# Kernel optimization log

Hardware: AMD Instinct MI355X
Metric: run time of the kernel (lower is better)

## Reference

```python
import jax, jax.numpy as jnp
import numpy as np

B, N = 65536, 8
OBS0, OBS1, OBS2 = 6, 1024, 7
H, HC, NA = 64, 128, 2


def _glorot(key, shape):
    fan_in = shape[0]
    lim = 1.0 / np.sqrt(fan_in)
    return jax.random.uniform(key, shape, jnp.float32, -lim, lim)


def setup_inputs() -> dict:
    key = jax.random.key(0)
    ks = jax.random.split(key, 24)
    state0 = jax.random.normal(ks[0], (B, OBS0), jnp.float32)
    state1 = jax.random.normal(ks[1], (B, OBS1), jnp.float32)
    state2 = jax.random.normal(ks[2], (B, N, OBS2), jnp.float32)
    keep = (jax.random.uniform(ks[3], (B, N, 1)) > 0.35) | (jnp.arange(N)[None, :, None] == 0)
    state2 = state2 * keep.astype(jnp.float32)
    return {
        "state0": state0, "state1": state1, "state2": state2,
        "W0": _glorot(ks[4], (OBS0, H)), "b0": jnp.zeros((H,), jnp.float32),
        "Wg": _glorot(ks[5], (OBS1, H)), "bg": jnp.zeros((H,), jnp.float32),
        "Ws1": _glorot(ks[6], (OBS2, H)), "bs1": jnp.zeros((H,), jnp.float32),
        "Ws2": _glorot(ks[7], (H, H)), "bs2": jnp.zeros((H,), jnp.float32),
        "Wq": _glorot(ks[8], (H, H)),
        "Wk": _glorot(ks[9], (H, H)),
        "Wv": _glorot(ks[10], (H, H)),
        "Wc1": _glorot(ks[11], (3 * H, HC)), "bc1": jnp.zeros((HC,), jnp.float32),
        "Wc2": _glorot(ks[12], (HC, HC)), "bc2": jnp.zeros((HC,), jnp.float32),
        "Wc3": _glorot(ks[13], (HC, NA)), "bc3": jnp.zeros((NA,), jnp.float32),
    }


def reference(state0, state1, state2,
              W0, b0, Wg, bg, Ws1, bs1, Ws2, bs2,
              Wq, Wk, Wv, Wc1, bc1, Wc2, bc2, Wc3, bc3):
    own_e = jax.nn.relu(state0 @ W0 + b0)                      # [B, 64]
    env_e = jax.nn.relu(state1 @ Wg + bg)                      # [B, 64]
    intru_e = jax.nn.relu(state2 @ Ws1 + bs1)                  # [B, N, 64]
    intru_e = jax.nn.relu(intru_e @ Ws2 + bs2)                 # [B, N, 64]

    q = own_e @ Wq                                             # [B, 64]
    k = intru_e @ Wk                                           # [B, N, 64]
    v = intru_e @ Wv                                           # [B, N, 64]

    # mask: True where the neighbor slot is non-padding (mean over feats != 0)
    mask = jnp.mean(state2, axis=2, keepdims=True) != 0        # [B, N, 1] bool

    score = jnp.einsum('bnd,bd->bn', k, q)[..., None]          # [B, N, 1]
    score_m = jnp.where(mask, score, -jnp.inf)
    alpha = jax.nn.softmax(score_m / np.sqrt(H), axis=1)       # [B, N, 1]
    alpha_m = jnp.where(mask, alpha, 0.0)
    v_att = jnp.sum(v * alpha_m, axis=1)                       # [B, 64]

    concat = jnp.concatenate((own_e, env_e, v_att), axis=1)    # [B, 192]
    h = jax.nn.relu(concat @ Wc1 + bc1)
    h = jax.nn.relu(h @ Wc2 + bc2)
    return jnp.tanh(h @ Wc3 + bc3)                             # [B, n_actions]
```

## Files before the change

### kernel.cpp

```cpp
#include <hip/hip_runtime.h>
#include <math.h>


typedef float f32x4 __attribute__((ext_vector_type(4)));
typedef __bf16 bf16x8 __attribute__((ext_vector_type(8)));
typedef unsigned short u16x8 __attribute__((ext_vector_type(8)));

#define DI __device__ __forceinline__

DI unsigned short f2bf_u(float f) {
  unsigned u = __builtin_bit_cast(unsigned, f);
  u += 0x7fffu + ((u >> 16) & 1u);
  return (unsigned short)(u >> 16);
}
DI float bfu2f(unsigned short s) {
  unsigned u = ((unsigned)s) << 16;
  return __builtin_bit_cast(float, u);
}
DI f32x4 mfma16(u16x8 a, u16x8 b, f32x4 c) {
  return __builtin_amdgcn_mfma_f32_16x16x32_bf16(
      __builtin_bit_cast(bf16x8, a), __builtin_bit_cast(bf16x8, b), c, 0, 0, 0);
}


constexpr size_t WS_ENV = 0;
constexpr size_t WS_WGF = 8388608;
constexpr size_t WS_WS2 = 8519680;
constexpr size_t WS_WV  = 8527872;
constexpr size_t WS_MQK = 8536064;
constexpr size_t WS_WC1 = 8544256;
constexpr size_t WS_WC2 = 8593408;
constexpr size_t WS_M32 = 8626176;

__global__ __launch_bounds__(256) void k_mqk(const float* __restrict__ Wq,
                                             const float* __restrict__ Wk,
                                             float* __restrict__ mqk) {
  const int idx = blockIdx.x * 256 + threadIdx.x;
  const int i = idx >> 6, h = idx & 63;
  const float* qp = Wq + i * 64;
  const float* kp = Wk + h * 64;
  float acc = 0.f;
#pragma unroll 16
  for (int d = 0; d < 64; ++d) acc = fmaf(qp[d], kp[d], acc);
  mqk[idx] = acc;
}

__global__ __launch_bounds__(256) void k_pack(
    const float* __restrict__ Wg, const float* __restrict__ Ws2,
    const float* __restrict__ Wv, const float* __restrict__ mqk,
    const float* __restrict__ Wc1, const float* __restrict__ Wc2,
    unsigned short* __restrict__ wgf, unsigned short* __restrict__ ws2f,
    unsigned short* __restrict__ wvf, unsigned short* __restrict__ mqkf,
    unsigned short* __restrict__ wc1f, unsigned short* __restrict__ wc2f) {
  const int idx = blockIdx.x * 256 + threadIdx.x;
  const float* src;
  unsigned short* dst;
  int i, ntm, NC;
  if (idx < 65536)      { src = Wg;  dst = wgf;  i = idx;          ntm = 2; NC = 64;  }
  else if (idx < 69632) { src = Ws2; dst = ws2f; i = idx - 65536;  ntm = 2; NC = 64;  }
  else if (idx < 73728) { src = Wv;  dst = wvf;  i = idx - 69632;  ntm = 2; NC = 64;  }
  else if (idx < 77824) { src = mqk; dst = mqkf; i = idx - 73728;  ntm = 2; NC = 64;  }
  else if (idx < 102400){ src = Wc1; dst = wc1f; i = idx - 77824;  ntm = 3; NC = 128; }
  else                  { src = Wc2; dst = wc2f; i = idx - 102400; ntm = 3; NC = 128; }
  const int j = i & 7, ln = (i >> 3) & 63, t2 = i >> 9;
  const int nt = t2 & ((1 << ntm) - 1), kt = t2 >> ntm;
  const int k = kt * 32 + (ln >> 4) * 8 + j, n = nt * 16 + (ln & 15);
  dst[i] = f2bf_u(src[k * NC + n]);
}

__global__ __launch_bounds__(256) void k_env(const float* __restrict__ s1,
                                             const float* __restrict__ bg,
                                             const unsigned short* __restrict__ wgf,
                                             unsigned short* __restrict__ env) {
  const int lane = threadIdx.x & 63, wave = threadIdx.x >> 6;
  const int lo = lane & 15, q = lane >> 4;
  const int row16 = blockIdx.x * 64 + wave * 16;
  const float* arow = s1 + (size_t)(row16 + lo) * 1024 + q * 8;
  const u16x8* wp = (const u16x8*)wgf + lane;

  f32x4 acc0 = {}, acc1 = {}, acc2 = {}, acc3 = {};
  f32x4 a0 = *(const f32x4*)(arow);
  f32x4 a1 = *(const f32x4*)(arow + 4);
  u16x8 b0 = wp[0], b1 = wp[64], b2 = wp[128], b3 = wp[192];

  for (int ks = 0; ks < 32; ++ks) {
    const f32x4 ca0 = a0, ca1 = a1;
    const u16x8 cb0 = b0, cb1 = b1, cb2 = b2, cb3 = b3;
    if (ks < 31) {
      const float* ap = arow + (ks + 1) * 32;
      a0 = *(const f32x4*)ap;
      a1 = *(const f32x4*)(ap + 4);
      const u16x8* bp = wp + (size_t)(ks + 1) * 256;
      b0 = bp[0]; b1 = bp[64]; b2 = bp[128]; b3 = bp[192];
    }
    u16x8 af;
    af[0] = f2bf_u(ca0[0]); af[1] = f2bf_u(ca0[1]);
    af[2] = f2bf_u(ca0[2]); af[3] = f2bf_u(ca0[3]);
    af[4] = f2bf_u(ca1[0]); af[5] = f2bf_u(ca1[1]);
    af[6] = f2bf_u(ca1[2]); af[7] = f2bf_u(ca1[3]);
    acc0 = mfma16(af, cb0, acc0);
    acc1 = mfma16(af, cb1, acc1);
    acc2 = mfma16(af, cb2, acc2);
    acc3 = mfma16(af, cb3, acc3);
  }
  const float bias[4] = {bg[lo], bg[16 + lo], bg[32 + lo], bg[48 + lo]};
  const f32x4 av[4] = {acc0, acc1, acc2, acc3};
#pragma unroll
  for (int nt = 0; nt < 4; ++nt)
#pragma unroll
    for (int ri = 0; ri < 4; ++ri) {
      float v = fmaxf(av[nt][ri] + bias[nt], 0.f);
      env[(size_t)(row16 + q * 4 + ri) * 64 + nt * 16 + lo] = f2bf_u(v);
    }
}

__global__ __launch_bounds__(256) void k_fused(
    const float* __restrict__ s0, const float* __restrict__ s2,
    const unsigned short* __restrict__ env,
    const float* __restrict__ W0, const float* __restrict__ b0v,
    const float* __restrict__ Ws1, const float* __restrict__ bs1,
    const unsigned short* __restrict__ ws2f, const float* __restrict__ bs2,
    const unsigned short* __restrict__ wvf, const unsigned short* __restrict__ mqkf,
    const unsigned short* __restrict__ wc1f, const float* __restrict__ bc1,
    const unsigned short* __restrict__ wc2f, const float* __restrict__ bc2,
    const float* __restrict__ Wc3, const float* __restrict__ bc3,
    float* __restrict__ out) {
  __shared__ __align__(16) char smem[55296];
  u16x8* EF = (u16x8*)smem;
  unsigned short* EFs = (unsigned short*)smem;
  u16x8* H1F = (u16x8*)smem;
  unsigned short* H1Fs = (unsigned short*)smem;
  float* H2 = (float*)(smem + 8192);
  u16x8* CF = (u16x8*)(smem + 32768);
  unsigned short* CFs = (unsigned short*)(smem + 32768);
  float* QK = (float*)(smem + 45056);
  u16x8* SEF = (u16x8*)(smem + 45056);
  float* SC = (float*)(smem + 53248);
  float* AL = (float*)(smem + 54272);

  const int tid = threadIdx.x;
  const int lane = tid & 63, wave = tid >> 6;
  const int lo = lane & 15, q = lane >> 4;
  const int bbase = blockIdx.x * 32;

  bool maskreg;
  {
    const int r = tid, bl = r >> 3, n = r & 7;
    const float* x = s2 + ((size_t)(bbase + bl) * 8 + n) * 7;
    float xv[7];
#pragma unroll
    for (int j = 0; j < 7; ++j) xv[j] = x[j];
    float sum = 0.f;
#pragma unroll
    for (int j = 0; j < 7; ++j) sum += xv[j];
    maskreg = (sum != 0.f);
    const int mt = r >> 4, rl = r & 15;
#pragma unroll
    for (int c = 0; c < 8; ++c) {
      float a[8];
#pragma unroll
      for (int i = 0; i < 8; ++i) a[i] = bs1[c * 8 + i];
#pragma unroll
      for (int j = 0; j < 7; ++j) {
        const float* wr = Ws1 + j * 64 + c * 8;
#pragma unroll
        for (int i = 0; i < 8; ++i) a[i] = fmaf(xv[j], wr[i], a[i]);
      }
      u16x8 pk;
#pragma unroll
      for (int i = 0; i < 8; ++i) pk[i] = f2bf_u(fmaxf(a[i], 0.f));
      EF[(mt * 2 + (c >> 2)) * 64 + (((c & 3) << 4) | rl)] = pk;
    }
  }
  __syncthreads();

  {
    u16x8 Bf[4][2];
#pragma unroll
    for (int nt = 0; nt < 4; ++nt)
#pragma unroll
      for (int kt = 0; kt < 2; ++kt)
        Bf[nt][kt] = ((const u16x8*)ws2f)[(kt * 4 + nt) * 64 + lane];
    float bias[4];
#pragma unroll
    for (int nt = 0; nt < 4; ++nt) bias[nt] = bs2[nt * 16 + lo];
#pragma unroll
    for (int mi = 0; mi < 4; ++mi) {
      const int mt = wave * 4 + mi;
      const u16x8 A0 = EF[(mt * 2 + 0) * 64 + lane];
      const u16x8 A1 = EF[(mt * 2 + 1) * 64 + lane];
      f32x4 acc[4] = {};
#pragma unroll
      for (int nt = 0; nt < 4; ++nt) {
        acc[nt] = mfma16(A0, Bf[nt][0], acc[nt]);
        acc[nt] = mfma16(A1, Bf[nt][1], acc[nt]);
      }
#pragma unroll
      for (int nt = 0; nt < 4; ++nt) {
        const int h = nt * 16 + lo;
#pragma unroll
        for (int ri = 0; ri < 4; ++ri) {
          const float v = fmaxf(acc[nt][ri] + bias[nt], 0.f);
          const int rr = mt * 16 + q * 4 + ri;
          EFs[((mt * 2 + (h >> 5)) * 64 + ((((h >> 3) & 3) << 4) | (rr & 15))) * 8 +
              (h & 7)] = f2bf_u(v);
        }
      }
    }
  }
  __syncthreads();

  {
    const int bl = tid >> 3, c = tid & 7;
    const int mt = bl >> 4, fl = ((c & 3) << 4) | (bl & 15), kt = c >> 2;
    const float* x = s0 + (size_t)(bbase + bl) * 6;
    float xv[6];
#pragma unroll
    for (int j = 0; j < 6; ++j) xv[j] = x[j];
    float a[8];
#pragma unroll
    for (int i = 0; i < 8; ++i) a[i] = b0v[c * 8 + i];
#pragma unroll
    for (int j = 0; j < 6; ++j) {
      const float* wr = W0 + j * 64 + c * 8;
#pragma unroll
      for (int i = 0; i < 8; ++i) a[i] = fmaf(xv[j], wr[i], a[i]);
    }
    u16x8 pk;
#pragma unroll
    for (int i = 0; i < 8; ++i) pk[i] = f2bf_u(fmaxf(a[i], 0.f));
    CF[(mt * 6 + kt) * 64 + fl] = pk;
    const u16x8 ev = *(const u16x8*)(env + (size_t)(bbase + bl) * 64 + c * 8);
    CF[(mt * 6 + 2 + kt) * 64 + fl] = ev;
  }
  __syncthreads();

  {
#pragma unroll
    for (int pp = 0; pp < 2; ++pp) {
      const int p = wave * 2 + pp, mt = p >> 2, nt = p & 3;
      const u16x8 A0 = CF[(mt * 6 + 0) * 64 + lane];
      const u16x8 A1 = CF[(mt * 6 + 1) * 64 + lane];
      const u16x8 B0 = ((const u16x8*)mqkf)[(0 * 4 + nt) * 64 + lane];
      const u16x8 B1 = ((const u16x8*)mqkf)[(1 * 4 + nt) * 64 + lane];
      f32x4 acc = {};
      acc = mfma16(A0, B0, acc);
      acc = mfma16(A1, B1, acc);
#pragma unroll
      for (int ri = 0; ri < 4; ++ri)
        QK[(mt * 16 + q * 4 + ri) * 64 + nt * 16 + lo] = acc[ri];
    }
  }
  __syncthreads();

  {
    const int r = tid, bl = r >> 3, mt = r >> 4, rl = r & 15;
    float dot = 0.f;
#pragma unroll
    for (int c = 0; c < 8; ++c) {
      const u16x8 e = EF[(mt * 2 + (c >> 2)) * 64 + (((c & 3) << 4) | rl)];
      const float* qkp = QK + bl * 64 + c * 8;
      const f32x4 qa = *(const f32x4*)(qkp);
      const f32x4 qb = *(const f32x4*)(qkp + 4);
#pragma unroll
      for (int i = 0; i < 4; ++i) dot = fmaf(bfu2f(e[i]), qa[i], dot);
#pragma unroll
      for (int i = 0; i < 4; ++i) dot = fmaf(bfu2f(e[4 + i]), qb[i], dot);
    }
    SC[r] = maskreg ? dot * 0.125f : -1e30f;
  }
  __syncthreads();

  if (tid < 32) {
    float s[8];
#pragma unroll
    for (int n = 0; n < 8; ++n) s[n] = SC[tid * 8 + n];
    float mx = s[0];
#pragma unroll
    for (int n = 1; n < 8; ++n) mx = fmaxf(mx, s[n]);
    float e[8], sum = 0.f;
#pragma unroll
    for (int n = 0; n < 8; ++n) { e[n] = __expf(s[n] - mx); sum += e[n]; }
    const float inv = 1.f / sum;
#pragma unroll
    for (int n = 0; n < 8; ++n) AL[tid * 8 + n] = e[n] * inv;
  }
  __syncthreads();

  {
    const int bl = tid >> 3, c = tid & 7;
    float al[8];
#pragma unroll
    for (int n = 0; n < 8; ++n) al[n] = AL[bl * 8 + n];
    float a[8] = {0.f, 0.f, 0.f, 0.f, 0.f, 0.f, 0.f, 0.f};
#pragma unroll
    for (int n = 0; n < 8; ++n) {
      const int rr = bl * 8 + n;
      const u16x8 e =
          EF[((rr >> 4) * 2 + (c >> 2)) * 64 + (((c & 3) << 4) | (rr & 15))];
#pragma unroll
      for (int i = 0; i < 8; ++i) a[i] = fmaf(al[n], bfu2f(e[i]), a[i]);
    }
    u16x8 pk;
#pragma unroll
    for (int i = 0; i < 8; ++i) pk[i] = f2bf_u(a[i]);
    SEF[((bl >> 4) * 2 + (c >> 2)) * 64 + (((c & 3) << 4) | (bl & 15))] = pk;
  }
  __syncthreads();

  {
#pragma unroll
    for (int pp = 0; pp < 2; ++pp) {
      const int p = wave * 2 + pp, mt = p >> 2, nt = p & 3;
      const u16x8 A0 = SEF[(mt * 2 + 0) * 64 + lane];
      const u16x8 A1 = SEF[(mt * 2 + 1) * 64 + lane];
      const u16x8 B0 = ((const u16x8*)wvf)[(0 * 4 + nt) * 64 + lane];
      const u16x8 B1 = ((const u16x8*)wvf)[(1 * 4 + nt) * 64 + lane];
      f32x4 acc = {};
      acc = mfma16(A0, B0, acc);
      acc = mfma16(A1, B1, acc);
      const int h = nt * 16 + lo;
#pragma unroll
      for (int ri = 0; ri < 4; ++ri) {
        const int rr = mt * 16 + q * 4 + ri;
        CFs[((mt * 6 + 4 + (h >> 5)) * 64 + ((((h >> 3) & 3) << 4) | (rr & 15))) * 8 +
            (h & 7)] = f2bf_u(acc[ri]);
      }
    }
  }
  __syncthreads();

  {
    const int mt = wave & 1, ntb = (wave >> 1) * 4;
    u16x8 A[6];
#pragma unroll
    for (int kt = 0; kt < 6; ++kt) A[kt] = CF[(mt * 6 + kt) * 64 + lane];
#pragma unroll
    for (int ni = 0; ni < 4; ++ni) {
      const int nt = ntb + ni;
      f32x4 acc = {};
#pragma unroll
      for (int kt = 0; kt < 6; ++kt) {
        const u16x8 Bf = ((const u16x8*)wc1f)[(kt * 8 + nt) * 64 + lane];
        acc = mfma16(A[kt], Bf, acc);
      }
      const float bias = bc1[nt * 16 + lo];
      const int h = nt * 16 + lo;
#pragma unroll
      for (int ri = 0; ri < 4; ++ri) {
        const float v = fmaxf(acc[ri] + bias, 0.f);
        const int rr = mt * 16 + q * 4 + ri;
        H1Fs[((mt * 4 + (h >> 5)) * 64 + ((((h >> 3) & 3) << 4) | (rr & 15))) * 8 +
             (h & 7)] = f2bf_u(v);
      }
    }
  }
  __syncthreads();

  {
    const int mt = wave & 1, ntb = (wave >> 1) * 4;
    u16x8 A[4];
#pragma unroll
    for (int kt = 0; kt < 4; ++kt) A[kt] = H1F[(mt * 4 + kt) * 64 + lane];
#pragma unroll
    for (int ni = 0; ni < 4; ++ni) {
      const int nt = ntb + ni;
      f32x4 acc = {};
#pragma unroll
      for (int kt = 0; kt < 4; ++kt) {
        const u16x8 Bf = ((const u16x8*)wc2f)[(kt * 8 + nt) * 64 + lane];
        acc = mfma16(A[kt], Bf, acc);
      }
      const float bias = bc2[nt * 16 + lo];
#pragma unroll
      for (int ri = 0; ri < 4; ++ri)
        H2[(mt * 16 + q * 4 + ri) * 132 + nt * 16 + lo] =
            fmaxf(acc[ri] + bias, 0.f);
    }
  }
  __syncthreads();

  if (tid < 64) {
    const int bl = tid >> 1, a = tid & 1;
    float acc = bc3[a];
    const float* h2r = H2 + bl * 132;
#pragma unroll 8
    for (int h = 0; h < 128; ++h) acc = fmaf(h2r[h], Wc3[h * 2 + a], acc);
    out[(size_t)(bbase + bl) * 2 + a] = tanhf(acc);
  }
}

extern "C" void kernel_launch(void* const* d_in, const int* in_sizes, int n_in,
                              void* d_out, int out_size, void* d_ws, size_t ws_size,
                              hipStream_t stream) {
  const float* s0  = (const float*)d_in[0];
  const float* s1  = (const float*)d_in[1];
  const float* s2  = (const float*)d_in[2];
  const float* W0  = (const float*)d_in[3];
  const float* b0  = (const float*)d_in[4];
  const float* Wg  = (const float*)d_in[5];
  const float* bg  = (const float*)d_in[6];
  const float* Ws1 = (const float*)d_in[7];
  const float* bs1 = (const float*)d_in[8];
  const float* Ws2 = (const float*)d_in[9];
  const float* bs2 = (const float*)d_in[10];
  const float* Wq  = (const float*)d_in[11];
  const float* Wk  = (const float*)d_in[12];
  const float* Wv  = (const float*)d_in[13];
  const float* Wc1 = (const float*)d_in[14];
  const float* bc1 = (const float*)d_in[15];
  const float* Wc2 = (const float*)d_in[16];
  const float* bc2 = (const float*)d_in[17];
  const float* Wc3 = (const float*)d_in[18];
  const float* bc3 = (const float*)d_in[19];

  char* ws = (char*)d_ws;
  unsigned short* env  = (unsigned short*)(ws + WS_ENV);
  unsigned short* wgf  = (unsigned short*)(ws + WS_WGF);
  unsigned short* ws2f = (unsigned short*)(ws + WS_WS2);
  unsigned short* wvf  = (unsigned short*)(ws + WS_WV);
  unsigned short* mqkf = (unsigned short*)(ws + WS_MQK);
  unsigned short* wc1f = (unsigned short*)(ws + WS_WC1);
  unsigned short* wc2f = (unsigned short*)(ws + WS_WC2);
  float* mqk32 = (float*)(ws + WS_M32);

  hipLaunchKernelGGL(k_mqk, dim3(16), dim3(256), 0, stream, Wq, Wk, mqk32);
  hipLaunchKernelGGL(k_pack, dim3(464), dim3(256), 0, stream, Wg, Ws2, Wv, mqk32,
                     Wc1, Wc2, wgf, ws2f, wvf, mqkf, wc1f, wc2f);
  hipLaunchKernelGGL(k_env, dim3(1024), dim3(256), 0, stream, s1, bg, wgf, env);
  hipLaunchKernelGGL(k_fused, dim3(2048), dim3(256), 0, stream, s0, s2, env, W0,
                     b0, Ws1, bs1, ws2f, bs2, wvf, mqkf, wc1f, bc1, wc2f, bc2,
                     Wc3, bc3, (float*)d_out);
}
```

Before: 496.6 us.

## Fuse env GEMM into main kernel and merge mqk into weight packing

Moves the state1 @ Wg GEMM into the main per-block kernel, split-K across wave pairs with a shared-memory reduction, so the bf16 env intermediate is never written to or read back from global memory. The Wq·Wk^T product is computed inside the packing kernel, which removes one launch. Inputs are loaded up front, and the final Wc3 projection now uses all threads with shuffle reductions. The cost is higher register pressure in the fused kernel (launch bounds set to 3 blocks per CU), plus an extra barrier and shared-memory reduction step.

```diff
diff --git a/kernel.cpp b/kernel.cpp
--- a/kernel.cpp
+++ b/kernel.cpp
@@ -3,6 +3,8 @@
 
 
 typedef float f32x4 __attribute__((ext_vector_type(4)));
+typedef float f32x4u __attribute__((ext_vector_type(4), aligned(4)));
+typedef float f32x2u __attribute__((ext_vector_type(2), aligned(4)));
 typedef __bf16 bf16x8 __attribute__((ext_vector_type(8)));
 typedef unsigned short u16x8 __attribute__((ext_vector_type(8)));
 
@@ -17,115 +19,79 @@
   unsigned u = ((unsigned)s) << 16;
   return __builtin_bit_cast(float, u);
 }
+DI u16x8 cvt8(f32x4 x, f32x4 y) {
+  bf16x8 r;
+  r[0] = (__bf16)x[0]; r[1] = (__bf16)x[1]; r[2] = (__bf16)x[2]; r[3] = (__bf16)x[3];
+  r[4] = (__bf16)y[0]; r[5] = (__bf16)y[1]; r[6] = (__bf16)y[2]; r[7] = (__bf16)y[3];
+  return __builtin_bit_cast(u16x8, r);
+}
 DI f32x4 mfma16(u16x8 a, u16x8 b, f32x4 c) {
   return __builtin_amdgcn_mfma_f32_16x16x32_bf16(
       __builtin_bit_cast(bf16x8, a), __builtin_bit_cast(bf16x8, b), c, 0, 0, 0);
 }
 
 
-constexpr size_t WS_ENV = 0;
-constexpr size_t WS_WGF = 8388608;
-constexpr size_t WS_WS2 = 8519680;
-constexpr size_t WS_WV  = 8527872;
-constexpr size_t WS_MQK = 8536064;
-constexpr size_t WS_WC1 = 8544256;
-constexpr size_t WS_WC2 = 8593408;
-constexpr size_t WS_M32 = 8626176;
-
-__global__ __launch_bounds__(256) void k_mqk(const float* __restrict__ Wq,
-                                             const float* __restrict__ Wk,
-                                             float* __restrict__ mqk) {
-  const int idx = blockIdx.x * 256 + threadIdx.x;
-  const int i = idx >> 6, h = idx & 63;
-  const float* qp = Wq + i * 64;
-  const float* kp = Wk + h * 64;
-  float acc = 0.f;
-#pragma unroll 16
-  for (int d = 0; d < 64; ++d) acc = fmaf(qp[d], kp[d], acc);
-  mqk[idx] = acc;
-}
-
-__global__ __launch_bounds__(256) void k_pack(
+constexpr size_t WS_WGF = 0;
+constexpr size_t WS_WS2 = 131072;
+constexpr size_t WS_WV  = 139264;
+constexpr size_t WS_MQK = 147456;
+constexpr size_t WS_WC1 = 155648;
+constexpr size_t WS_WC2 = 204800;
+
+__global__ __launch_bounds__(256) void k_prep(
     const float* __restrict__ Wg, const float* __restrict__ Ws2,
-    const float* __restrict__ Wv, const float* __restrict__ mqk,
-    const float* __restrict__ Wc1, const float* __restrict__ Wc2,
+    const float* __restrict__ Wv, const float* __restrict__ Wq,
+    const float* __restrict__ Wk, const float* __restrict__ Wc1,
+    const float* __restrict__ Wc2,
     unsigned short* __restrict__ wgf, unsigned short* __restrict__ ws2f,
     unsigned short* __restrict__ wvf, unsigned short* __restrict__ mqkf,
     unsigned short* __restrict__ wc1f, unsigned short* __restrict__ wc2f) {
   const int idx = blockIdx.x * 256 + threadIdx.x;
-  const float* src;
+  const float* src = nullptr;
   unsigned short* dst;
   int i, ntm, NC;
+  bool is_mqk = false;
   if (idx < 65536)      { src = Wg;  dst = wgf;  i = idx;          ntm = 2; NC = 64;  }
   else if (idx < 69632) { src = Ws2; dst = ws2f; i = idx - 65536;  ntm = 2; NC = 64;  }
   else if (idx < 73728) { src = Wv;  dst = wvf;  i = idx - 69632;  ntm = 2; NC = 64;  }
-  else if (idx < 77824) { src = mqk; dst = mqkf; i = idx - 73728;  ntm = 2; NC = 64;  }
+  else if (idx < 77824) { is_mqk = true; dst = mqkf; i = idx - 73728; ntm = 2; NC = 64; }
   else if (idx < 102400){ src = Wc1; dst = wc1f; i = idx - 77824;  ntm = 3; NC = 128; }
   else                  { src = Wc2; dst = wc2f; i = idx - 102400; ntm = 3; NC = 128; }
   const int j = i & 7, ln = (i >> 3) & 63, t2 = i >> 9;
   const int nt = t2 & ((1 << ntm) - 1), kt = t2 >> ntm;
   const int k = kt * 32 + (ln >> 4) * 8 + j, n = nt * 16 + (ln & 15);
-  dst[i] = f2bf_u(src[k * NC + n]);
-}
-
-__global__ __launch_bounds__(256) void k_env(const float* __restrict__ s1,
-                                             const float* __restrict__ bg,
-                                             const unsigned short* __restrict__ wgf,
-                                             unsigned short* __restrict__ env) {
-  const int lane = threadIdx.x & 63, wave = threadIdx.x >> 6;
-  const int lo = lane & 15, q = lane >> 4;
-  const int row16 = blockIdx.x * 64 + wave * 16;
-  const float* arow = s1 + (size_t)(row16 + lo) * 1024 + q * 8;
-  const u16x8* wp = (const u16x8*)wgf + lane;
-
-  f32x4 acc0 = {}, acc1 = {}, acc2 = {}, acc3 = {};
-  f32x4 a0 = *(const f32x4*)(arow);
-  f32x4 a1 = *(const f32x4*)(arow + 4);
-  u16x8 b0 = wp[0], b1 = wp[64], b2 = wp[128], b3 = wp[192];
-
-  for (int ks = 0; ks < 32; ++ks) {
-    const f32x4 ca0 = a0, ca1 = a1;
-    const u16x8 cb0 = b0, cb1 = b1, cb2 = b2, cb3 = b3;
-    if (ks < 31) {
-      const float* ap = arow + (ks + 1) * 32;
-      a0 = *(const f32x4*)ap;
-      a1 = *(const f32x4*)(ap + 4);
-      const u16x8* bp = wp + (size_t)(ks + 1) * 256;
-      b0 = bp[0]; b1 = bp[64]; b2 = bp[128]; b3 = bp[192];
-    }
-    u16x8 af;
-    af[0] = f2bf_u(ca0[0]); af[1] = f2bf_u(ca0[1]);
-    af[2] = f2bf_u(ca0[2]); af[3] = f2bf_u(ca0[3]);
-    af[4] = f2bf_u(ca1[0]); af[5] = f2bf_u(ca1[1]);
-    af[6] = f2bf_u(ca1[2]); af[7] = f2bf_u(ca1[3]);
-    acc0 = mfma16(af, cb0, acc0);
-    acc1 = mfma16(af, cb1, acc1);
-    acc2 = mfma16(af, cb2, acc2);
-    acc3 = mfma16(af, cb3, acc3);
-  }
-  const float bias[4] = {bg[lo], bg[16 + lo], bg[32 + lo], bg[48 + lo]};
-  const f32x4 av[4] = {acc0, acc1, acc2, acc3};
-#pragma unroll
-  for (int nt = 0; nt < 4; ++nt)
-#pragma unroll
-    for (int ri = 0; ri < 4; ++ri) {
-      float v = fmaxf(av[nt][ri] + bias[nt], 0.f);
-      env[(size_t)(row16 + q * 4 + ri) * 64 + nt * 16 + lo] = f2bf_u(v);
-    }
-}
-
-__global__ __launch_bounds__(256) void k_fused(
-    const float* __restrict__ s0, const float* __restrict__ s2,
-    const unsigned short* __restrict__ env,
+  float val;
+  if (is_mqk) {
+    const f32x4* qp = (const f32x4*)(Wq + k * 64);
+    const f32x4* kp = (const f32x4*)(Wk + n * 64);
+    float acc = 0.f;
+#pragma unroll
+    for (int d4 = 0; d4 < 16; ++d4) {
+      const f32x4 a = qp[d4], b = kp[d4];
+#pragma unroll
+      for (int e = 0; e < 4; ++e) acc = fmaf(a[e], b[e], acc);
+    }
+    val = acc;
+  } else {
+    val = src[k * NC + n];
+  }
+  dst[i] = f2bf_u(val);
+}
+
+__global__ __launch_bounds__(256, 3) void k_main(
+    const float* __restrict__ s0, const float* __restrict__ s1,
+    const float* __restrict__ s2,
     const float* __restrict__ W0, const float* __restrict__ b0v,
+    const float* __restrict__ bg,
     const float* __restrict__ Ws1, const float* __restrict__ bs1,
     const unsigned short* __restrict__ ws2f, const float* __restrict__ bs2,
     const unsigned short* __restrict__ wvf, const unsigned short* __restrict__ mqkf,
     const unsigned short* __restrict__ wc1f, const float* __restrict__ bc1,
     const unsigned short* __restrict__ wc2f, const float* __restrict__ bc2,
     const float* __restrict__ Wc3, const float* __restrict__ bc3,
+    const unsigned short* __restrict__ wgf,
     float* __restrict__ out) {
-  __shared__ __align__(16) char smem[55296];
+  __shared__ __align__(16) char smem[54272];
   u16x8* EF = (u16x8*)smem;
   unsigned short* EFs = (unsigned short*)smem;
   u16x8* H1F = (u16x8*)smem;
@@ -134,27 +100,81 @@
   u16x8* CF = (u16x8*)(smem + 32768);
   unsigned short* CFs = (unsigned short*)(smem + 32768);
   float* QK = (float*)(smem + 45056);
+  f32x4* RED4 = (f32x4*)(smem + 45056);
   u16x8* SEF = (u16x8*)(smem + 45056);
   float* SC = (float*)(smem + 53248);
-  float* AL = (float*)(smem + 54272);
 
   const int tid = threadIdx.x;
   const int lane = tid & 63, wave = tid >> 6;
   const int lo = lane & 15, q = lane >> 4;
   const int bbase = blockIdx.x * 32;
 
+  const int bl8 = tid >> 3, n8 = tid & 7;
+  const float* s2p = s2 + ((size_t)(bbase + bl8) * 8 + n8) * 7;
+  const f32x4u x03 = *(const f32x4u*)s2p;
+  const f32x2u x45 = *(const f32x2u*)(s2p + 4);
+  const float x6 = s2p[6];
+  const float* s0p = s0 + (size_t)(bbase + bl8) * 6;
+  const f32x4u y03 = *(const f32x4u*)s0p;
+  const f32x2u y45 = *(const f32x2u*)(s0p + 4);
+
+  const int p = wave & 1, emt = wave >> 1;
+  {
+    const float* arow =
+        s1 + (size_t)(bbase + emt * 16 + lo) * 1024 + p * 512 + q * 8;
+    const u16x8* wp = (const u16x8*)wgf + p * 4096 + lane;
+    f32x4 acc0 = {}, acc1 = {}, acc2 = {}, acc3 = {};
+    f32x4 a0 = *(const f32x4*)arow, a1 = *(const f32x4*)(arow + 4);
+    u16x8 b0 = wp[0], b1 = wp[64], b2 = wp[128], b3 = wp[192];
+    for (int ks = 0; ks < 16; ++ks) {
+      const f32x4 ca0 = a0, ca1 = a1;
+      const u16x8 cb0 = b0, cb1 = b1, cb2 = b2, cb3 = b3;
+      if (ks < 15) {
+        const float* ap = arow + (ks + 1) * 32;
+        a0 = *(const f32x4*)ap;
+        a1 = *(const f32x4*)(ap + 4);
+        const u16x8* bp = wp + (ks + 1) * 256;
+        b0 = bp[0]; b1 = bp[64]; b2 = bp[128]; b3 = bp[192];
+      }
+      const u16x8 af = cvt8(ca0, ca1);
+      acc0 = mfma16(af, cb0, acc0);
+      acc1 = mfma16(af, cb1, acc1);
+      acc2 = mfma16(af, cb2, acc2);
+      acc3 = mfma16(af, cb3, acc3);
+    }
+    if (p) {
+      RED4[0 * 128 + emt * 64 + lane] = acc0;
+      RED4[1 * 128 + emt * 64 + lane] = acc1;
+      RED4[2 * 128 + emt * 64 + lane] = acc2;
+      RED4[3 * 128 + emt * 64 + lane] = acc3;
+    }
+    __syncthreads();
+    if (!p) {
+      acc0 += RED4[0 * 128 + emt * 64 + lane];
+      acc1 += RED4[1 * 128 + emt * 64 + lane];
+      acc2 += RED4[2 * 128 + emt * 64 + lane];
+      acc3 += RED4[3 * 128 + emt * 64 + lane];
+      const f32x4 av[4] = {acc0, acc1, acc2, acc3};
+#pragma unroll
+      for (int nt = 0; nt < 4; ++nt) {
+        const float bias = bg[nt * 16 + lo];
+        const int h = nt * 16 + lo;
+#pragma unroll
+        for (int ri = 0; ri < 4; ++ri) {
+          const float v = fmaxf(av[nt][ri] + bias, 0.f);
+          CFs[((emt * 6 + 2 + (h >> 5)) * 64 +
+               ((((h >> 3) & 3) << 4) | (q * 4 + ri))) * 8 + (h & 7)] = f2bf_u(v);
+        }
+      }
+    }
+  }
+
   bool maskreg;
   {
-    const int r = tid, bl = r >> 3, n = r & 7;
-    const float* x = s2 + ((size_t)(bbase + bl) * 8 + n) * 7;
-    float xv[7];
-#pragma unroll
-    for (int j = 0; j < 7; ++j) xv[j] = x[j];
-    float sum = 0.f;
-#pragma unroll
-    for (int j = 0; j < 7; ++j) sum += xv[j];
+    float xv[7] = {x03[0], x03[1], x03[2], x03[3], x45[0], x45[1], x6};
+    const float sum = xv[0] + xv[1] + xv[2] + xv[3] + xv[4] + xv[5] + xv[6];
     maskreg = (sum != 0.f);
-    const int mt = r >> 4, rl = r & 15;
+    const int mt = tid >> 4, rl = tid & 15;
 #pragma unroll
     for (int c = 0; c < 8; ++c) {
       float a[8];
@@ -211,34 +231,28 @@
   __syncthreads();
 
   {
-    const int bl = tid >> 3, c = tid & 7;
-    const int mt = bl >> 4, fl = ((c & 3) << 4) | (bl & 15), kt = c >> 2;
-    const float* x = s0 + (size_t)(bbase + bl) * 6;
-    float xv[6];
-#pragma unroll
-    for (int j = 0; j < 6; ++j) xv[j] = x[j];
+    const int mt = bl8 >> 4, fl = ((n8 & 3) << 4) | (bl8 & 15), kt = n8 >> 2;
+    const float yv[6] = {y03[0], y03[1], y03[2], y03[3], y45[0], y45[1]};
     float a[8];
 #pragma unroll
-    for (int i = 0; i < 8; ++i) a[i] = b0v[c * 8 + i];
+    for (int i = 0; i < 8; ++i) a[i] = b0v[n8 * 8 + i];
 #pragma unroll
     for (int j = 0; j < 6; ++j) {
-      const float* wr = W0 + j * 64 + c * 8;
-#pragma unroll
-      for (int i = 0; i < 8; ++i) a[i] = fmaf(xv[j], wr[i], a[i]);
+      const float* wr = W0 + j * 64 + n8 * 8;
+#pragma unroll
+      for (int i = 0; i < 8; ++i) a[i] = fmaf(yv[j], wr[i], a[i]);
     }
     u16x8 pk;
 #pragma unroll
     for (int i = 0; i < 8; ++i) pk[i] = f2bf_u(fmaxf(a[i], 0.f));
     CF[(mt * 6 + kt) * 64 + fl] = pk;
-    const u16x8 ev = *(const u16x8*)(env + (size_t)(bbase + bl) * 64 + c * 8);
-    CF[(mt * 6 + 2 + kt) * 64 + fl] = ev;
   }
   __syncthreads();
 
   {
 #pragma unroll
     for (int pp = 0; pp < 2; ++pp) {
-      const int p = wave * 2 + pp, mt = p >> 2, nt = p & 3;
+      const int pr = wave * 2 + pp, mt = pr >> 2, nt = pr & 3;
       const u16x8 A0 = CF[(mt * 6 + 0) * 64 + lane];
       const u16x8 A1 = CF[(mt * 6 + 1) * 64 + lane];
       const u16x8 B0 = ((const u16x8*)mqkf)[(0 * 4 + nt) * 64 + lane];
@@ -283,35 +297,34 @@
     for (int n = 0; n < 8; ++n) { e[n] = __expf(s[n] - mx); sum += e[n]; }
     const float inv = 1.f / sum;
 #pragma unroll
-    for (int n = 0; n < 8; ++n) AL[tid * 8 + n] = e[n] * inv;
-  }
-  __syncthreads();
-
-  {
-    const int bl = tid >> 3, c = tid & 7;
+    for (int n = 0; n < 8; ++n) SC[tid * 8 + n] = e[n] * inv;
+  }
+  __syncthreads();
+
+  {
     float al[8];
 #pragma unroll
-    for (int n = 0; n < 8; ++n) al[n] = AL[bl * 8 + n];
+    for (int n = 0; n < 8; ++n) al[n] = SC[bl8 * 8 + n];
     float a[8] = {0.f, 0.f, 0.f, 0.f, 0.f, 0.f, 0.f, 0.f};
 #pragma unroll
     for (int n = 0; n < 8; ++n) {
-      const int rr = bl * 8 + n;
+      const int rr = bl8 * 8 + n;
       const u16x8 e =
-          EF[((rr >> 4) * 2 + (c >> 2)) * 64 + (((c & 3) << 4) | (rr & 15))];
+          EF[((rr >> 4) * 2 + (n8 >> 2)) * 64 + (((n8 & 3) << 4) | (rr & 15))];
 #pragma unroll
       for (int i = 0; i < 8; ++i) a[i] = fmaf(al[n], bfu2f(e[i]), a[i]);
     }
     u16x8 pk;
 #pragma unroll
     for (int i = 0; i < 8; ++i) pk[i] = f2bf_u(a[i]);
-    SEF[((bl >> 4) * 2 + (c >> 2)) * 64 + (((c & 3) << 4) | (bl & 15))] = pk;
+    SEF[((bl8 >> 4) * 2 + (n8 >> 2)) * 64 + (((n8 & 3) << 4) | (bl8 & 15))] = pk;
   }
   __syncthreads();
 
   {
 #pragma unroll
     for (int pp = 0; pp < 2; ++pp) {
-      const int p = wave * 2 + pp, mt = p >> 2, nt = p & 3;
+      const int pr = wave * 2 + pp, mt = pr >> 2, nt = pr & 3;
       const u16x8 A0 = SEF[(mt * 2 + 0) * 64 + lane];
       const u16x8 A1 = SEF[(mt * 2 + 1) * 64 + lane];
       const u16x8 B0 = ((const u16x8*)wvf)[(0 * 4 + nt) * 64 + lane];
@@ -380,13 +393,20 @@
   }
   __syncthreads();
 
-  if (tid < 64) {
-    const int bl = tid >> 1, a = tid & 1;
-    float acc = bc3[a];
-    const float* h2r = H2 + bl * 132;
-#pragma unroll 8
-    for (int h = 0; h < 128; ++h) acc = fmaf(h2r[h], Wc3[h * 2 + a], acc);
-    out[(size_t)(bbase + bl) * 2 + a] = tanhf(acc);
+  {
+    const int kq = n8 >> 1, a = n8 & 1;
+    const f32x4* h4 = (const f32x4*)(H2 + bl8 * 132 + kq * 32);
+    const float* wr = Wc3 + kq * 64;
+    float acc = 0.f;
+#pragma unroll
+    for (int j4 = 0; j4 < 8; ++j4) {
+      const f32x4 hv = h4[j4];
+#pragma unroll
+      for (int e = 0; e < 4; ++e) acc = fmaf(hv[e], wr[(j4 * 4 + e) * 2 + a], acc);
+    }
+    acc += __shfl_down(acc, 2);
+    acc += __shfl_down(acc, 4);
+    if (kq == 0) out[(size_t)(bbase + bl8) * 2 + a] = tanhf(acc + bc3[a]);
   }
 }
 
@@ -415,20 +435,16 @@
   const float* bc3 = (const float*)d_in[19];
 
   char* ws = (char*)d_ws;
-  unsigned short* env  = (unsigned short*)(ws + WS_ENV);
   unsigned short* wgf  = (unsigned short*)(ws + WS_WGF);
   unsigned short* ws2f = (unsigned short*)(ws + WS_WS2);
   unsigned short* wvf  = (unsigned short*)(ws + WS_WV);
   unsigned short* mqkf = (unsigned short*)(ws + WS_MQK);
   unsigned short* wc1f = (unsigned short*)(ws + WS_WC1);
   unsigned short* wc2f = (unsigned short*)(ws + WS_WC2);
-  float* mqk32 = (float*)(ws + WS_M32);
-
-  hipLaunchKernelGGL(k_mqk, dim3(16), dim3(256), 0, stream, Wq, Wk, mqk32);
-  hipLaunchKernelGGL(k_pack, dim3(464), dim3(256), 0, stream, Wg, Ws2, Wv, mqk32,
-                     Wc1, Wc2, wgf, ws2f, wvf, mqkf, wc1f, wc2f);
-  hipLaunchKernelGGL(k_env, dim3(1024), dim3(256), 0, stream, s1, bg, wgf, env);
-  hipLaunchKernelGGL(k_fused, dim3(2048), dim3(256), 0, stream, s0, s2, env, W0,
-                     b0, Ws1, bs1, ws2f, bs2, wvf, mqkf, wc1f, bc1, wc2f, bc2,
-                     Wc3, bc3, (float*)d_out);
-}
+
+  hipLaunchKernelGGL(k_prep, dim3(464), dim3(256), 0, stream, Wg, Ws2, Wv, Wq,
+                     Wk, Wc1, Wc2, wgf, ws2f, wvf, mqkf, wc1f, wc2f);
+  hipLaunchKernelGGL(k_main, dim3(2048), dim3(256), 0, stream, s0, s1, s2, W0,
+                     b0, bg, Ws1, bs1, ws2f, bs2, wvf, mqkf, wc1f, bc1, wc2f,
+                     bc2, Wc3, bc3, wgf, (float*)d_out);
+}
```

After: 460.2 us. 1.08x faster.
